# Optimization experiments

Hardware: AMD Instinct MI355X
Metric: run time of the kernel (lower is better)

## Reference

```python
import jax, jax.numpy as jnp
from jax import lax
import numpy as np

B, CIN, COUT, D, TDIM, E = 2, 16, 8, 96, 256, 8


def setup_inputs() -> dict:
    key = jax.random.key(0)
    ks = jax.random.split(key, 12)
    s = lambda fan: 1.0 / np.sqrt(fan)
    return {
        "x": jax.random.normal(ks[0], (B, CIN, D, D, D), jnp.float32),
        "text_features": jax.random.normal(ks[1], (B, TDIM), jnp.float32),
        # expert weight basis [E, Cout, Cin, 3, 3, 3] (kaiming-uniform-ish)
        "weight_basis": jax.random.uniform(ks[2], (E, COUT, CIN, 3, 3, 3), jnp.float32, -s(CIN * 27), s(CIN * 27)),
        "bias_basis": jnp.zeros((E, COUT), jnp.float32),
        # router MLP: text_dim -> 64 -> E
        "r_w1": jax.random.uniform(ks[3], (TDIM, 64), jnp.float32, -s(TDIM), s(TDIM)),
        "r_b1": jax.random.uniform(ks[4], (64,), jnp.float32, -s(TDIM), s(TDIM)),
        "r_w2": jax.random.uniform(ks[5], (64, E), jnp.float32, -s(64), s(64)),
        "r_b2": jax.random.uniform(ks[6], (E,), jnp.float32, -s(64), s(64)),
        # modulator MLP: text_dim -> 64 -> Cout
        "m_w1": jax.random.uniform(ks[7], (TDIM, 64), jnp.float32, -s(TDIM), s(TDIM)),
        "m_b1": jax.random.uniform(ks[8], (64,), jnp.float32, -s(TDIM), s(TDIM)),
        "m_w2": jax.random.uniform(ks[9], (64, COUT), jnp.float32, -s(64), s(64)),
        "m_b2": jax.random.uniform(ks[10], (COUT,), jnp.float32, -s(64), s(64)),
    }


def reference(x, text_features, weight_basis, bias_basis,
              r_w1, r_b1, r_w2, r_b2, m_w1, m_b1, m_w2, m_b2):
    b, cin = x.shape[0], x.shape[1]
    cout = weight_basis.shape[1]
    # router -> softmax routing weights over experts
    h = jax.nn.leaky_relu(text_features @ r_w1 + r_b1, 0.1)
    router_logits = h @ r_w2 + r_b2                      # [b, E]
    routing_weights = jax.nn.softmax(router_logits, -1)  # [b, E]
    # modulator -> per-sample channel gates
    g = jax.nn.leaky_relu(text_features @ m_w1 + m_b1, 0.1)
    gamma = jax.nn.sigmoid(g @ m_w2 + m_b2)              # [b, Cout]
    # per-sample dynamic conv weights via expert mixing
    cw = jnp.einsum('be,eoixyz->boixyz', routing_weights, weight_basis)  # [b,Cout,Cin,3,3,3]
    cb = routing_weights @ bias_basis                                    # [b, Cout]
    # grouped-conv trick: batch folded into channels, groups=b
    xr = x.reshape(1, b * cin, *x.shape[2:])
    wr = cw.reshape(b * cout, cin, 3, 3, 3)
    out = lax.conv_general_dilated(
        xr, wr, window_strides=(1, 1, 1), padding=[(1, 1)] * 3,
        dimension_numbers=('NCDHW', 'OIDHW', 'NCDHW'), feature_group_count=b)
    out = out.reshape(b, cout, *out.shape[2:]) + cb[:, :, None, None, None]
    out = out * (1.0 + gamma[:, :, None, None, None])
    return out, router_logits, routing_weights
```

## Files before the change

### kernel.cpp

```cpp
#include <hip/hip_runtime.h>
#include <math.h>

#define NB 2
#define CIN 16
#define COUT 8
#define DD 96
#define TDIM 256
#define NE 8
#define VOX (DD*DD*DD)
#define OUT_ELEMS (NB*COUT*VOX)

#define XT_BYTES ((size_t)NB * VOX * 32)
#define WS_A_F 7168
#define WS_D_F 7184

#define LX 18
#define PLANE (LX*LX)
#define NVX (PLANE*5)
#define HALFB (NVX*16)

#define NTB3 (VOX/512)

#define MWN (COUT*CIN*27)

typedef _Float16 f16x8 __attribute__((ext_vector_type(8)));
typedef _Float16 f16x4 __attribute__((ext_vector_type(4)));
typedef float f32x4 __attribute__((ext_vector_type(4)));

__global__ __launch_bounds__(256) void transpose_setup(
    const float* __restrict__ x, _Float16* __restrict__ xt,
    const float* __restrict__ text,
    const float* __restrict__ wb,
    const float* __restrict__ bb,
    const float* __restrict__ rw1, const float* __restrict__ rb1,
    const float* __restrict__ rw2, const float* __restrict__ rb2,
    const float* __restrict__ mw1, const float* __restrict__ mb1,
    const float* __restrict__ mw2, const float* __restrict__ mb2,
    float* __restrict__ dout_tail,
    char* __restrict__ tab)
{
    __shared__ struct {
        float mw[MWN];
        float part[256];
        float hg[2][64];
        float logits[NE];
        float rwv[NE];
    } s;
    const int t = threadIdx.x;
    const int b = blockIdx.y;

    if (blockIdx.x == NTB3) {
        {
            const int o = t & 127;
            const int which = o >> 6, j = o & 63;
            const int kh = t >> 7;
            const float* __restrict__ w1 = which ? mw1 : rw1;
            const float* __restrict__ tx = text + b*TDIM + kh*128;
            const float* __restrict__ wp = w1 + (size_t)(kh*128)*64 + j;
            float a0 = 0.f, a1 = 0.f, a2 = 0.f, a3 = 0.f;
            #pragma unroll 8
            for (int k = 0; k < 128; k += 4) {
                a0 = fmaf(tx[k+0], wp[(k+0)*64], a0);
                a1 = fmaf(tx[k+1], wp[(k+1)*64], a1);
                a2 = fmaf(tx[k+2], wp[(k+2)*64], a2);
                a3 = fmaf(tx[k+3], wp[(k+3)*64], a3);
            }
            s.part[t] = (a0 + a1) + (a2 + a3);
        }
        __syncthreads();
        if (t < 128) {
            const int which = t >> 6, j = t & 63;
            float acc = (which ? mb1 : rb1)[j] + s.part[t] + s.part[t + 128];
            s.hg[which][j] = (acc >= 0.f) ? acc : 0.1f * acc;
        }
        __syncthreads();
        if (t < NE) {
            float acc = rb2[t];
            #pragma unroll
            for (int k = 0; k < 64; ++k) acc = fmaf(s.hg[0][k], rw2[k*NE + t], acc);
            s.logits[t] = acc;
            dout_tail[b*NE + t] = acc;
        }
        __syncthreads();
        if (t < NE) {
            float mx = s.logits[0];
            for (int k = 1; k < NE; ++k) mx = fmaxf(mx, s.logits[k]);
            float ssum = 0.f;
            for (int k = 0; k < NE; ++k) ssum += expf(s.logits[k] - mx);
            const float w = expf(s.logits[t] - mx) / ssum;
            s.rwv[t] = w;
            dout_tail[NB*NE + b*NE + t] = w;
        }
        __syncthreads();
        float rv[NE];
        #pragma unroll
        for (int e = 0; e < NE; ++e) rv[e] = s.rwv[e];

        if (t < COUT) {
            float acc = mb2[t];
            #pragma unroll
            for (int k = 0; k < 64; ++k) acc = fmaf(s.hg[1][k], mw2[k*COUT + t], acc);
            const float gamma = 1.f / (1.f + expf(-acc));
            const float a = 1.f + gamma;
            float cb = 0.f;
            #pragma unroll
            for (int e = 0; e < NE; ++e) cb = fmaf(rv[e], bb[e*COUT + t], cb);
            ((float*)tab)[WS_A_F + b*COUT + t] = a;
            ((float*)tab)[WS_D_F + b*COUT + t] = cb * a;
        }

        #pragma unroll
        for (int i0 = 0; i0 < (MWN + 255)/256; ++i0) {
            const int i = i0*256 + t;
            if (i < MWN) {
                float v = 0.f;
                #pragma unroll
                for (int e = 0; e < NE; ++e) v = fmaf(rv[e], wb[e*MWN + i], v);
                s.mw[i] = v;
            }
        }
        __syncthreads();

        for (int r = t; r < 14*64*8; r += 256) {
            const int c  = r >> 9;
            const int l  = (r >> 3) & 63;
            const int j  = r & 7;
            const int q  = l >> 4;
            const int n  = l & 15;
            const int p  = q & 1;
            const int ci = (q >> 1)*8 + j;
            int tap;
            if (c < 9)        tap = (c/3)*9 + (c%3)*3 + p;
            else if (c < 12)  tap = (c-9)*9 + p*3 + 2;
            else if (c == 12) tap = p*9 + 8;
            else              tap = p ? -1 : 26;
            float v = 0.f;
            if (n < 8 && tap >= 0) v = s.mw[(n*CIN + ci)*27 + tap];
            ((_Float16*)tab)[b*7168 + r] = (_Float16)v;
        }
        return;
    }

    const int vh = blockIdx.x * 256 + t;
    const float* __restrict__ xb = x + (size_t)b * CIN * VOX;

    float2 f[CIN];
    #pragma unroll
    for (int ci = 0; ci < CIN; ++ci)
        f[ci] = ((const float2*)(xb + (size_t)ci * VOX))[vh];

    union { _Float16 h[16]; uint4 u[2]; } o0, o1;
    #pragma unroll
    for (int ci = 0; ci < CIN; ++ci) {
        o0.h[ci] = (_Float16)f[ci].x;
        o1.h[ci] = (_Float16)f[ci].y;
    }

    uint4* __restrict__ dst = (uint4*)(xt + (size_t)b * VOX * 16) + (size_t)vh * 4;
    dst[0] = o0.u[0];
    dst[1] = o0.u[1];
    dst[2] = o1.u[0];
    dst[3] = o1.u[1];
}

__global__ __launch_bounds__(256) void conv_mfma(
    const _Float16* __restrict__ xt,
    const char* __restrict__ tab,
    float* __restrict__ out)
{
    __shared__ char lds[2*HALFB];
    const int tid  = threadIdx.x;
    const int lane = tid & 63;
    const int wv   = tid >> 6;
    const int b    = blockIdx.z;
    const int z0   = blockIdx.y * 3;
    const int xti  = blockIdx.x % 6;
    const int yti  = blockIdx.x / 6;
    const int x0   = xti * 16, y0 = yti * 16;

    const f16x8* __restrict__ bfp = (const f16x8*)tab;
    f16x8 bfrag[14];
    #pragma unroll
    for (int c = 0; c < 14; ++c)
        bfrag[c] = bfp[(b*14 + c)*64 + lane];

    const _Float16* __restrict__ xtb = xt + (size_t)b * VOX * 16;
    for (int sv = tid; sv < NVX; sv += 256) {
        const int lz = sv / PLANE;
        const int r1 = sv - lz * PLANE;
        const int ly = r1 / LX;
        const int lx = r1 - ly * LX;
        const int zg = z0 - 1 + lz, yg = y0 - 1 + ly, xg = x0 - 1 + lx;
        const bool ok = ((unsigned)zg < 96u) & ((unsigned)yg < 96u) & ((unsigned)xg < 96u);
        const int zc = ok ? zg : 0, yc = ok ? yg : 0, xc = ok ? xg : 0;
        const uint4* __restrict__ p = (const uint4*)(xtb + (size_t)((zc*DD + yc)*DD + xc) * 16);
        uint4 lo = {0,0,0,0}, hi = {0,0,0,0};
        if (ok) { lo = p[0]; hi = p[1]; }
        *(uint4*)&lds[sv*16]         = lo;
        *(uint4*)&lds[HALFB + sv*16] = hi;
    }
    __syncthreads();

    const int q    = lane >> 4;
    const int m    = lane & 15;
    const int pbit = q & 1;
    const int hbit = q >> 1;

    const float* tabf = (const float*)tab;
    const float a_n = tabf[WS_A_F + b*8 + (m & 7)];
    const float d_n = tabf[WS_D_F + b*8 + (m & 7)];

    const int com = hbit*HALFB + m*16;
    const int dA = pbit*16;
    const int dB = pbit*288;
    const int dC = pbit*5184;

    #define LD_A(p_, dy_)  (*(const f16x8*)&lds[((p_)*PLANE + (yi+(dy_))*LX)*16 + com + dA])
    #define LD_G(p_)       (*(const f16x8*)&lds[((p_)*PLANE + yi*LX + 2)*16 + com + dB])
    #define LD_H12(zi_)    (*(const f16x8*)&lds[((zi_)*PLANE + (yi+2)*LX + 2)*16 + com + dC])
    #define LD_H13(zi_)    (*(const f16x8*)&lds[(((zi_)+2)*PLANE + (yi+2)*LX + 2)*16 + com])

    #pragma unroll
    for (int yi4 = 0; yi4 < 4; ++yi4) {
        const int yi = wv*4 + yi4;

        f16x8 A[3][3], G[3];
        #pragma unroll
        for (int dy = 0; dy < 3; ++dy) { A[0][dy] = LD_A(0, dy); A[1][dy] = LD_A(1, dy); }
        G[0] = LD_G(0); G[1] = LD_G(1);

        #pragma unroll
        for (int zi = 0; zi < 3; ++zi) {
            #pragma unroll
            for (int dy = 0; dy < 3; ++dy) A[2][dy] = LD_A(zi+2, dy);
            G[2] = LD_G(zi+2);
            const f16x8 H12v = LD_H12(zi);
            const f16x8 H13v = LD_H13(zi);

            f32x4 acc0 = {0.f,0.f,0.f,0.f}, acc1 = {0.f,0.f,0.f,0.f};
            acc0 = __builtin_amdgcn_mfma_f32_16x16x32_f16(A[0][0], bfrag[0],  acc0, 0,0,0);
            acc1 = __builtin_amdgcn_mfma_f32_16x16x32_f16(A[0][1], bfrag[1],  acc1, 0,0,0);
            acc0 = __builtin_amdgcn_mfma_f32_16x16x32_f16(A[0][2], bfrag[2],  acc0, 0,0,0);
            acc1 = __builtin_amdgcn_mfma_f32_16x16x32_f16(A[1][0], bfrag[3],  acc1, 0,0,0);
            acc0 = __builtin_amdgcn_mfma_f32_16x16x32_f16(A[1][1], bfrag[4],  acc0, 0,0,0);
            acc1 = __builtin_amdgcn_mfma_f32_16x16x32_f16(A[1][2], bfrag[5],  acc1, 0,0,0);
            acc0 = __builtin_amdgcn_mfma_f32_16x16x32_f16(A[2][0], bfrag[6],  acc0, 0,0,0);
            acc1 = __builtin_amdgcn_mfma_f32_16x16x32_f16(A[2][1], bfrag[7],  acc1, 0,0,0);
            acc0 = __builtin_amdgcn_mfma_f32_16x16x32_f16(A[2][2], bfrag[8],  acc0, 0,0,0);
            acc1 = __builtin_amdgcn_mfma_f32_16x16x32_f16(G[0],    bfrag[9],  acc1, 0,0,0);
            acc0 = __builtin_amdgcn_mfma_f32_16x16x32_f16(G[1],    bfrag[10], acc0, 0,0,0);
            acc1 = __builtin_amdgcn_mfma_f32_16x16x32_f16(G[2],    bfrag[11], acc1, 0,0,0);
            acc0 = __builtin_amdgcn_mfma_f32_16x16x32_f16(H12v,    bfrag[12], acc0, 0,0,0);
            acc1 = __builtin_amdgcn_mfma_f32_16x16x32_f16(H13v,    bfrag[13], acc1, 0,0,0);

            if (m < 8) {
                const int zz = z0 + zi, yy = y0 + yi;
                float* __restrict__ op = out + (size_t)(b*COUT + m)*VOX
                                            + (size_t)(zz*DD + yy)*DD + x0 + q*4;
                f32x4 res;
                #pragma unroll
                for (int r = 0; r < 4; ++r) res[r] = fmaf(acc0[r] + acc1[r], a_n, d_n);
                *reinterpret_cast<f32x4*>(op) = res;
            }

            #pragma unroll
            for (int dy = 0; dy < 3; ++dy) { A[0][dy] = A[1][dy]; A[1][dy] = A[2][dy]; }
            G[0] = G[1]; G[1] = G[2];
        }
    }
    #undef LD_A
    #undef LD_G
    #undef LD_H12
    #undef LD_H13
}

extern "C" void kernel_launch(void* const* d_in, const int* in_sizes, int n_in,
                              void* d_out, int out_size, void* d_ws, size_t ws_size,
                              hipStream_t stream) {
    const float* x    = (const float*)d_in[0];
    const float* text = (const float*)d_in[1];
    const float* wb   = (const float*)d_in[2];
    const float* bb   = (const float*)d_in[3];
    const float* rw1  = (const float*)d_in[4];
    const float* rb1  = (const float*)d_in[5];
    const float* rw2  = (const float*)d_in[6];
    const float* rb2  = (const float*)d_in[7];
    const float* mw1  = (const float*)d_in[8];
    const float* mb1  = (const float*)d_in[9];
    const float* mw2  = (const float*)d_in[10];
    const float* mb2  = (const float*)d_in[11];

    float* out = (float*)d_out;
    _Float16* xt = (_Float16*)d_ws;
    char* tab = (char*)d_ws + XT_BYTES;

    transpose_setup<<<dim3(NTB3 + 1, NB), 256, 0, stream>>>(
        x, xt, text, wb, bb, rw1, rb1, rw2, rb2, mw1, mb1, mw2, mb2,
        out + OUT_ELEMS, tab);

    conv_mfma<<<dim3(36, 32, NB), 256, 0, stream>>>(xt, tab, out);
}
```

Baseline: 249.7 us.

## Stream z-planes through an LDS ring buffer and fold the router into the conv kernel

The conv kernel now processes 12 output z-slices per block instead of 3. It keeps a 5-plane ring buffer in LDS, prefetching the next input plane into registers while computing the current one, which cuts halo reloads from 5 planes per 3 outputs to about 14 per 12. The router/modulator MLP and expert weight mixing move into every conv block, computed redundantly in LDS, so the separate setup block and the workspace table go away. The trade-off is a fixed per-block prologue (MLP plus mixing of about 27K weights), less parallelism from 4x fewer blocks, and a launch-bounds occupancy hint.

Result: no change. 252.2 us (+1.0%).

```diff
diff --git a/kernel.cpp b/kernel.cpp
--- a/kernel.cpp
+++ b/kernel.cpp
@@ -10,25 +10,48 @@
 #define VOX (DD*DD*DD)
 #define OUT_ELEMS (NB*COUT*VOX)
 
-#define XT_BYTES ((size_t)NB * VOX * 32)
-#define WS_A_F 7168
-#define WS_D_F 7184
-
 #define LX 18
 #define PLANE (LX*LX)
-#define NVX (PLANE*5)
+#define RING 5
+#define NVX (PLANE*RING)
 #define HALFB (NVX*16)
+#define ZCH 12
+#define NZB (DD/ZCH)
 
 #define NTB3 (VOX/512)
-
 #define MWN (COUT*CIN*27)
 
 typedef _Float16 f16x8 __attribute__((ext_vector_type(8)));
-typedef _Float16 f16x4 __attribute__((ext_vector_type(4)));
 typedef float f32x4 __attribute__((ext_vector_type(4)));
 
-__global__ __launch_bounds__(256) void transpose_setup(
-    const float* __restrict__ x, _Float16* __restrict__ xt,
+__global__ __launch_bounds__(256) void transpose_k(
+    const float* __restrict__ x, _Float16* __restrict__ xt)
+{
+    const int t = threadIdx.x;
+    const int b = blockIdx.y;
+    const int vh = blockIdx.x * 256 + t;
+    const float* __restrict__ xb = x + (size_t)b * CIN * VOX;
+
+    float2 f[CIN];
+    #pragma unroll
+    for (int ci = 0; ci < CIN; ++ci)
+        f[ci] = ((const float2*)(xb + (size_t)ci * VOX))[vh];
+
+    union { _Float16 h[16]; uint4 u[2]; } o0, o1;
+    #pragma unroll
+    for (int ci = 0; ci < CIN; ++ci) {
+        o0.h[ci] = (_Float16)f[ci].x;
+        o1.h[ci] = (_Float16)f[ci].y;
+    }
+    uint4* __restrict__ dst = (uint4*)(xt + (size_t)b * VOX * 16) + (size_t)vh * 4;
+    dst[0] = o0.u[0];
+    dst[1] = o0.u[1];
+    dst[2] = o1.u[0];
+    dst[3] = o1.u[1];
+}
+
+__global__ __launch_bounds__(256, 3) void conv_mfma(
+    const _Float16* __restrict__ xt,
     const float* __restrict__ text,
     const float* __restrict__ wb,
     const float* __restrict__ bb,
@@ -37,135 +60,6 @@
     const float* __restrict__ mw1, const float* __restrict__ mb1,
     const float* __restrict__ mw2, const float* __restrict__ mb2,
     float* __restrict__ dout_tail,
-    char* __restrict__ tab)
-{
-    __shared__ struct {
-        float mw[MWN];
-        float part[256];
-        float hg[2][64];
-        float logits[NE];
-        float rwv[NE];
-    } s;
-    const int t = threadIdx.x;
-    const int b = blockIdx.y;
-
-    if (blockIdx.x == NTB3) {
-        {
-            const int o = t & 127;
-            const int which = o >> 6, j = o & 63;
-            const int kh = t >> 7;
-            const float* __restrict__ w1 = which ? mw1 : rw1;
-            const float* __restrict__ tx = text + b*TDIM + kh*128;
-            const float* __restrict__ wp = w1 + (size_t)(kh*128)*64 + j;
-            float a0 = 0.f, a1 = 0.f, a2 = 0.f, a3 = 0.f;
-            #pragma unroll 8
-            for (int k = 0; k < 128; k += 4) {
-                a0 = fmaf(tx[k+0], wp[(k+0)*64], a0);
-                a1 = fmaf(tx[k+1], wp[(k+1)*64], a1);
-                a2 = fmaf(tx[k+2], wp[(k+2)*64], a2);
-                a3 = fmaf(tx[k+3], wp[(k+3)*64], a3);
-            }
-            s.part[t] = (a0 + a1) + (a2 + a3);
-        }
-        __syncthreads();
-        if (t < 128) {
-            const int which = t >> 6, j = t & 63;
-            float acc = (which ? mb1 : rb1)[j] + s.part[t] + s.part[t + 128];
-            s.hg[which][j] = (acc >= 0.f) ? acc : 0.1f * acc;
-        }
-        __syncthreads();
-        if (t < NE) {
-            float acc = rb2[t];
-            #pragma unroll
-            for (int k = 0; k < 64; ++k) acc = fmaf(s.hg[0][k], rw2[k*NE + t], acc);
-            s.logits[t] = acc;
-            dout_tail[b*NE + t] = acc;
-        }
-        __syncthreads();
-        if (t < NE) {
-            float mx = s.logits[0];
-            for (int k = 1; k < NE; ++k) mx = fmaxf(mx, s.logits[k]);
-            float ssum = 0.f;
-            for (int k = 0; k < NE; ++k) ssum += expf(s.logits[k] - mx);
-            const float w = expf(s.logits[t] - mx) / ssum;
-            s.rwv[t] = w;
-            dout_tail[NB*NE + b*NE + t] = w;
-        }
-        __syncthreads();
-        float rv[NE];
-        #pragma unroll
-        for (int e = 0; e < NE; ++e) rv[e] = s.rwv[e];
-
-        if (t < COUT) {
-            float acc = mb2[t];
-            #pragma unroll
-            for (int k = 0; k < 64; ++k) acc = fmaf(s.hg[1][k], mw2[k*COUT + t], acc);
-            const float gamma = 1.f / (1.f + expf(-acc));
-            const float a = 1.f + gamma;
-            float cb = 0.f;
-            #pragma unroll
-            for (int e = 0; e < NE; ++e) cb = fmaf(rv[e], bb[e*COUT + t], cb);
-            ((float*)tab)[WS_A_F + b*COUT + t] = a;
-            ((float*)tab)[WS_D_F + b*COUT + t] = cb * a;
-        }
-
-        #pragma unroll
-        for (int i0 = 0; i0 < (MWN + 255)/256; ++i0) {
-            const int i = i0*256 + t;
-            if (i < MWN) {
-                float v = 0.f;
-                #pragma unroll
-                for (int e = 0; e < NE; ++e) v = fmaf(rv[e], wb[e*MWN + i], v);
-                s.mw[i] = v;
-            }
-        }
-        __syncthreads();
-
-        for (int r = t; r < 14*64*8; r += 256) {
-            const int c  = r >> 9;
-            const int l  = (r >> 3) & 63;
-            const int j  = r & 7;
-            const int q  = l >> 4;
-            const int n  = l & 15;
-            const int p  = q & 1;
-            const int ci = (q >> 1)*8 + j;
-            int tap;
-            if (c < 9)        tap = (c/3)*9 + (c%3)*3 + p;
-            else if (c < 12)  tap = (c-9)*9 + p*3 + 2;
-            else if (c == 12) tap = p*9 + 8;
-            else              tap = p ? -1 : 26;
-            float v = 0.f;
-            if (n < 8 && tap >= 0) v = s.mw[(n*CIN + ci)*27 + tap];
-            ((_Float16*)tab)[b*7168 + r] = (_Float16)v;
-        }
-        return;
-    }
-
-    const int vh = blockIdx.x * 256 + t;
-    const float* __restrict__ xb = x + (size_t)b * CIN * VOX;
-
-    float2 f[CIN];
-    #pragma unroll
-    for (int ci = 0; ci < CIN; ++ci)
-        f[ci] = ((const float2*)(xb + (size_t)ci * VOX))[vh];
-
-    union { _Float16 h[16]; uint4 u[2]; } o0, o1;
-    #pragma unroll
-    for (int ci = 0; ci < CIN; ++ci) {
-        o0.h[ci] = (_Float16)f[ci].x;
-        o1.h[ci] = (_Float16)f[ci].y;
-    }
-
-    uint4* __restrict__ dst = (uint4*)(xt + (size_t)b * VOX * 16) + (size_t)vh * 4;
-    dst[0] = o0.u[0];
-    dst[1] = o0.u[1];
-    dst[2] = o1.u[0];
-    dst[3] = o1.u[1];
-}
-
-__global__ __launch_bounds__(256) void conv_mfma(
-    const _Float16* __restrict__ xt,
-    const char* __restrict__ tab,
     float* __restrict__ out)
 {
     __shared__ char lds[2*HALFB];
@@ -173,88 +67,189 @@
     const int lane = tid & 63;
     const int wv   = tid >> 6;
     const int b    = blockIdx.z;
-    const int z0   = blockIdx.y * 3;
+    const int zb   = blockIdx.y * ZCH;
     const int xti  = blockIdx.x % 6;
     const int yti  = blockIdx.x / 6;
     const int x0   = xti * 16, y0 = yti * 16;
-
-    const f16x8* __restrict__ bfp = (const f16x8*)tab;
+    const bool wr  = (blockIdx.x == 0) && (blockIdx.y == 0);
+
+    float* smw   = (float*)lds;
+    float* spart = (float*)(lds + 13824);
+    float* shg   = (float*)(lds + 14848);
+    float* slog  = (float*)(lds + 15360);
+    float* srwv  = (float*)(lds + 15392);
+    float* sa    = (float*)(lds + 15424);
+    float* sd    = (float*)(lds + 15456);
+
+    {
+        const int o = tid & 127, which = o >> 6, j = o & 63, kh = tid >> 7;
+        const float* __restrict__ w1 = which ? mw1 : rw1;
+        const float* __restrict__ tx = text + b*TDIM + kh*128;
+        const float* __restrict__ wp = w1 + (size_t)(kh*128)*64 + j;
+        float a0=0.f, a1=0.f, a2=0.f, a3=0.f;
+        #pragma unroll 8
+        for (int k = 0; k < 128; k += 4) {
+            a0 = fmaf(tx[k+0], wp[(k+0)*64], a0);
+            a1 = fmaf(tx[k+1], wp[(k+1)*64], a1);
+            a2 = fmaf(tx[k+2], wp[(k+2)*64], a2);
+            a3 = fmaf(tx[k+3], wp[(k+3)*64], a3);
+        }
+        spart[tid] = (a0 + a1) + (a2 + a3);
+    }
+    __syncthreads();
+    if (tid < 128) {
+        const int which = tid >> 6, j = tid & 63;
+        float acc = (which ? mb1 : rb1)[j] + spart[tid] + spart[tid + 128];
+        shg[which*64 + j] = (acc >= 0.f) ? acc : 0.1f * acc;
+    }
+    __syncthreads();
+    if (tid < NE) {
+        float acc = rb2[tid];
+        #pragma unroll
+        for (int k = 0; k < 64; ++k) acc = fmaf(shg[k], rw2[k*NE + tid], acc);
+        slog[tid] = acc;
+        if (wr) dout_tail[b*NE + tid] = acc;
+    }
+    __syncthreads();
+    if (tid < NE) {
+        float mx = slog[0];
+        for (int k = 1; k < NE; ++k) mx = fmaxf(mx, slog[k]);
+        float ssum = 0.f;
+        for (int k = 0; k < NE; ++k) ssum += expf(slog[k] - mx);
+        const float w = expf(slog[tid] - mx) / ssum;
+        srwv[tid] = w;
+        if (wr) dout_tail[NB*NE + b*NE + tid] = w;
+    }
+    __syncthreads();
+    float rv[NE];
+    #pragma unroll
+    for (int e = 0; e < NE; ++e) rv[e] = srwv[e];
+    if (tid < COUT) {
+        float acc = mb2[tid];
+        #pragma unroll
+        for (int k = 0; k < 64; ++k) acc = fmaf(shg[64 + k], mw2[k*COUT + tid], acc);
+        const float gamma = 1.f / (1.f + expf(-acc));
+        const float a = 1.f + gamma;
+        float cb = 0.f;
+        #pragma unroll
+        for (int e = 0; e < NE; ++e) cb = fmaf(rv[e], bb[e*COUT + tid], cb);
+        sa[tid] = a;
+        sd[tid] = cb * a;
+    }
+    #pragma unroll
+    for (int i0 = 0; i0 < (MWN + 255)/256; ++i0) {
+        const int i = i0*256 + tid;
+        if (i < MWN) {
+            float v = 0.f;
+            #pragma unroll
+            for (int e = 0; e < NE; ++e) v = fmaf(rv[e], wb[e*MWN + i], v);
+            smw[i] = v;
+        }
+    }
+    __syncthreads();
+
+    const int q = lane >> 4, m = lane & 15, pbit = q & 1, hbit = q >> 1;
     f16x8 bfrag[14];
-    #pragma unroll
-    for (int c = 0; c < 14; ++c)
-        bfrag[c] = bfp[(b*14 + c)*64 + lane];
+    {
+        const int cib = (q >> 1) * 8;
+        #pragma unroll
+        for (int c = 0; c < 14; ++c) {
+            int tap;
+            if (c < 9)        tap = (c/3)*9 + (c%3)*3 + pbit;
+            else if (c < 12)  tap = (c-9)*9 + pbit*3 + 2;
+            else if (c == 12) tap = pbit*9 + 8;
+            else              tap = pbit ? -1 : 26;
+            f16x8 v;
+            #pragma unroll
+            for (int j = 0; j < 8; ++j) v[j] = (_Float16)0.f;
+            if (m < 8 && tap >= 0) {
+                const float* mr = smw + (m*CIN + cib)*27 + tap;
+                #pragma unroll
+                for (int j = 0; j < 8; ++j) v[j] = (_Float16)mr[j*27];
+            }
+            bfrag[c] = v;
+        }
+    }
+    const float a_n = sa[m & 7];
+    const float d_n = sd[m & 7];
+    __syncthreads();
 
     const _Float16* __restrict__ xtb = xt + (size_t)b * VOX * 16;
-    for (int sv = tid; sv < NVX; sv += 256) {
-        const int lz = sv / PLANE;
-        const int r1 = sv - lz * PLANE;
-        const int ly = r1 / LX;
-        const int lx = r1 - ly * LX;
-        const int zg = z0 - 1 + lz, yg = y0 - 1 + ly, xg = x0 - 1 + lx;
-        const bool ok = ((unsigned)zg < 96u) & ((unsigned)yg < 96u) & ((unsigned)xg < 96u);
-        const int zc = ok ? zg : 0, yc = ok ? yg : 0, xc = ok ? xg : 0;
-        const uint4* __restrict__ p = (const uint4*)(xtb + (size_t)((zc*DD + yc)*DD + xc) * 16);
-        uint4 lo = {0,0,0,0}, hi = {0,0,0,0};
-        if (ok) { lo = p[0]; hi = p[1]; }
-        *(uint4*)&lds[sv*16]         = lo;
-        *(uint4*)&lds[HALFB + sv*16] = hi;
-    }
-    __syncthreads();
-
-    const int q    = lane >> 4;
-    const int m    = lane & 15;
-    const int pbit = q & 1;
-    const int hbit = q >> 1;
-
-    const float* tabf = (const float*)tab;
-    const float a_n = tabf[WS_A_F + b*8 + (m & 7)];
-    const float d_n = tabf[WS_D_F + b*8 + (m & 7)];
+    const int lyA = tid / LX, lxA = tid - lyA*LX;
+    const int ygA = y0 - 1 + lyA, xgA = x0 - 1 + lxA;
+    const bool okA = ((unsigned)ygA < 96u) & ((unsigned)xgA < 96u);
+    const int pvA = ygA*DD + xgA;
+    const int sB  = tid + 256;
+    const bool hasB = sB < PLANE;
+    const int lyB = sB / LX, lxB = sB - lyB*LX;
+    const int ygB = y0 - 1 + lyB, xgB = x0 - 1 + lxB;
+    const bool okB = hasB && (((unsigned)ygB < 96u) & ((unsigned)xgB < 96u));
+    const int pvB = ygB*DD + xgB;
+
+    #pragma unroll
+    for (int lp = 0; lp < 4; ++lp) {
+        const int zg = zb - 1 + lp;
+        const bool zok = (unsigned)zg < 96u;
+        uint4 l0 = make_uint4(0,0,0,0), h0 = l0, l1 = l0, h1 = l0;
+        if (okA && zok) { const uint4* p = (const uint4*)(xtb + ((size_t)zg*(DD*DD) + pvA)*16); l0 = p[0]; h0 = p[1]; }
+        if (okB && zok) { const uint4* p = (const uint4*)(xtb + ((size_t)zg*(DD*DD) + pvB)*16); l1 = p[0]; h1 = p[1]; }
+        *(uint4*)&lds[(lp*PLANE + tid)*16]          = l0;
+        *(uint4*)&lds[HALFB + (lp*PLANE + tid)*16]  = h0;
+        if (hasB) {
+            *(uint4*)&lds[(lp*PLANE + sB)*16]         = l1;
+            *(uint4*)&lds[HALFB + (lp*PLANE + sB)*16] = h1;
+        }
+    }
+    __syncthreads();
 
     const int com = hbit*HALFB + m*16;
     const int dA = pbit*16;
-    const int dB = pbit*288;
-    const int dC = pbit*5184;
-
-    #define LD_A(p_, dy_)  (*(const f16x8*)&lds[((p_)*PLANE + (yi+(dy_))*LX)*16 + com + dA])
-    #define LD_G(p_)       (*(const f16x8*)&lds[((p_)*PLANE + yi*LX + 2)*16 + com + dB])
-    #define LD_H12(zi_)    (*(const f16x8*)&lds[((zi_)*PLANE + (yi+2)*LX + 2)*16 + com + dC])
-    #define LD_H13(zi_)    (*(const f16x8*)&lds[(((zi_)+2)*PLANE + (yi+2)*LX + 2)*16 + com])
-
-    #pragma unroll
-    for (int yi4 = 0; yi4 < 4; ++yi4) {
-        const int yi = wv*4 + yi4;
-
-        f16x8 A[3][3], G[3];
-        #pragma unroll
-        for (int dy = 0; dy < 3; ++dy) { A[0][dy] = LD_A(0, dy); A[1][dy] = LD_A(1, dy); }
-        G[0] = LD_G(0); G[1] = LD_G(1);
-
-        #pragma unroll
-        for (int zi = 0; zi < 3; ++zi) {
-            #pragma unroll
-            for (int dy = 0; dy < 3; ++dy) A[2][dy] = LD_A(zi+2, dy);
-            G[2] = LD_G(zi+2);
-            const f16x8 H12v = LD_H12(zi);
-            const f16x8 H13v = LD_H13(zi);
+    const int dB = pbit*(LX*16);
+
+    #define LDV(sl_, vo_, dd_) (*(const f16x8*)&lds[((sl_)*PLANE + (vo_))*16 + com + (dd_)])
+
+    for (int zo = 0; zo < ZCH; ++zo) {
+        const bool st = (zo <= ZCH-3);
+        const int zgs = zb + zo + 3;
+        uint4 l0 = make_uint4(0,0,0,0), h0 = l0, l1 = l0, h1 = l0;
+        if (st) {
+            const bool zok = (unsigned)zgs < 96u;
+            if (okA && zok) { const uint4* p = (const uint4*)(xtb + ((size_t)zgs*(DD*DD) + pvA)*16); l0 = p[0]; h0 = p[1]; }
+            if (okB && zok) { const uint4* p = (const uint4*)(xtb + ((size_t)zgs*(DD*DD) + pvB)*16); l1 = p[0]; h1 = p[1]; }
+        }
+
+        const int s_0 = zo % RING, s_1 = (zo+1) % RING, s_2 = (zo+2) % RING;
+        const int sH12 = pbit ? s_1 : s_0;
+        const int sl0 = s_0, sl1 = s_1, sl2 = s_2;
+
+        #pragma unroll
+        for (int yi4 = 0; yi4 < 4; ++yi4) {
+            const int yi = wv*4 + yi4;
+            const f16x8 A00 = LDV(sl0, (yi+0)*LX, dA), A01 = LDV(sl0, (yi+1)*LX, dA), A02 = LDV(sl0, (yi+2)*LX, dA);
+            const f16x8 A10 = LDV(sl1, (yi+0)*LX, dA), A11 = LDV(sl1, (yi+1)*LX, dA), A12 = LDV(sl1, (yi+2)*LX, dA);
+            const f16x8 A20 = LDV(sl2, (yi+0)*LX, dA), A21 = LDV(sl2, (yi+1)*LX, dA), A22 = LDV(sl2, (yi+2)*LX, dA);
+            const f16x8 G0  = LDV(sl0, yi*LX + 2, dB), G1  = LDV(sl1, yi*LX + 2, dB), G2  = LDV(sl2, yi*LX + 2, dB);
+            const f16x8 H12v = LDV(sH12, (yi+2)*LX + 2, 0);
+            const f16x8 H13v = LDV(sl2,  (yi+2)*LX + 2, 0);
 
             f32x4 acc0 = {0.f,0.f,0.f,0.f}, acc1 = {0.f,0.f,0.f,0.f};
-            acc0 = __builtin_amdgcn_mfma_f32_16x16x32_f16(A[0][0], bfrag[0],  acc0, 0,0,0);
-            acc1 = __builtin_amdgcn_mfma_f32_16x16x32_f16(A[0][1], bfrag[1],  acc1, 0,0,0);
-            acc0 = __builtin_amdgcn_mfma_f32_16x16x32_f16(A[0][2], bfrag[2],  acc0, 0,0,0);
-            acc1 = __builtin_amdgcn_mfma_f32_16x16x32_f16(A[1][0], bfrag[3],  acc1, 0,0,0);
-            acc0 = __builtin_amdgcn_mfma_f32_16x16x32_f16(A[1][1], bfrag[4],  acc0, 0,0,0);
-            acc1 = __builtin_amdgcn_mfma_f32_16x16x32_f16(A[1][2], bfrag[5],  acc1, 0,0,0);
-            acc0 = __builtin_amdgcn_mfma_f32_16x16x32_f16(A[2][0], bfrag[6],  acc0, 0,0,0);
-            acc1 = __builtin_amdgcn_mfma_f32_16x16x32_f16(A[2][1], bfrag[7],  acc1, 0,0,0);
-            acc0 = __builtin_amdgcn_mfma_f32_16x16x32_f16(A[2][2], bfrag[8],  acc0, 0,0,0);
-            acc1 = __builtin_amdgcn_mfma_f32_16x16x32_f16(G[0],    bfrag[9],  acc1, 0,0,0);
-            acc0 = __builtin_amdgcn_mfma_f32_16x16x32_f16(G[1],    bfrag[10], acc0, 0,0,0);
-            acc1 = __builtin_amdgcn_mfma_f32_16x16x32_f16(G[2],    bfrag[11], acc1, 0,0,0);
-            acc0 = __builtin_amdgcn_mfma_f32_16x16x32_f16(H12v,    bfrag[12], acc0, 0,0,0);
-            acc1 = __builtin_amdgcn_mfma_f32_16x16x32_f16(H13v,    bfrag[13], acc1, 0,0,0);
+            acc0 = __builtin_amdgcn_mfma_f32_16x16x32_f16(A00,  bfrag[0],  acc0, 0,0,0);
+            acc1 = __builtin_amdgcn_mfma_f32_16x16x32_f16(A01,  bfrag[1],  acc1, 0,0,0);
+            acc0 = __builtin_amdgcn_mfma_f32_16x16x32_f16(A02,  bfrag[2],  acc0, 0,0,0);
+            acc1 = __builtin_amdgcn_mfma_f32_16x16x32_f16(A10,  bfrag[3],  acc1, 0,0,0);
+            acc0 = __builtin_amdgcn_mfma_f32_16x16x32_f16(A11,  bfrag[4],  acc0, 0,0,0);
+            acc1 = __builtin_amdgcn_mfma_f32_16x16x32_f16(A12,  bfrag[5],  acc1, 0,0,0);
+            acc0 = __builtin_amdgcn_mfma_f32_16x16x32_f16(A20,  bfrag[6],  acc0, 0,0,0);
+            acc1 = __builtin_amdgcn_mfma_f32_16x16x32_f16(A21,  bfrag[7],  acc1, 0,0,0);
+            acc0 = __builtin_amdgcn_mfma_f32_16x16x32_f16(A22,  bfrag[8],  acc0, 0,0,0);
+            acc1 = __builtin_amdgcn_mfma_f32_16x16x32_f16(G0,   bfrag[9],  acc1, 0,0,0);
+            acc0 = __builtin_amdgcn_mfma_f32_16x16x32_f16(G1,   bfrag[10], acc0, 0,0,0);
+            acc1 = __builtin_amdgcn_mfma_f32_16x16x32_f16(G2,   bfrag[11], acc1, 0,0,0);
+            acc0 = __builtin_amdgcn_mfma_f32_16x16x32_f16(H12v, bfrag[12], acc0, 0,0,0);
+            acc1 = __builtin_amdgcn_mfma_f32_16x16x32_f16(H13v, bfrag[13], acc1, 0,0,0);
 
             if (m < 8) {
-                const int zz = z0 + zi, yy = y0 + yi;
+                const int zz = zb + zo, yy = y0 + yi;
                 float* __restrict__ op = out + (size_t)(b*COUT + m)*VOX
                                             + (size_t)(zz*DD + yy)*DD + x0 + q*4;
                 f32x4 res;
@@ -262,16 +257,20 @@
                 for (int r = 0; r < 4; ++r) res[r] = fmaf(acc0[r] + acc1[r], a_n, d_n);
                 *reinterpret_cast<f32x4*>(op) = res;
             }
-
-            #pragma unroll
-            for (int dy = 0; dy < 3; ++dy) { A[0][dy] = A[1][dy]; A[1][dy] = A[2][dy]; }
-            G[0] = G[1]; G[1] = G[2];
-        }
-    }
-    #undef LD_A
-    #undef LD_G
-    #undef LD_H12
-    #undef LD_H13
+        }
+
+        if (st) {
+            const int sls = (zo+4) % RING;
+            *(uint4*)&lds[(sls*PLANE + tid)*16]          = l0;
+            *(uint4*)&lds[HALFB + (sls*PLANE + tid)*16]  = h0;
+            if (hasB) {
+                *(uint4*)&lds[(sls*PLANE + sB)*16]         = l1;
+                *(uint4*)&lds[HALFB + (sls*PLANE + sB)*16] = h1;
+            }
+        }
+        __syncthreads();
+    }
+    #undef LDV
 }
 
 extern "C" void kernel_launch(void* const* d_in, const int* in_sizes, int n_in,
@@ -292,11 +291,10 @@
 
     float* out = (float*)d_out;
     _Float16* xt = (_Float16*)d_ws;
-    char* tab = (char*)d_ws + XT_BYTES;
-
-    transpose_setup<<<dim3(NTB3 + 1, NB), 256, 0, stream>>>(
-        x, xt, text, wb, bb, rw1, rb1, rw2, rb2, mw1, mb1, mw2, mb2,
-        out + OUT_ELEMS, tab);
-
-    conv_mfma<<<dim3(36, 32, NB), 256, 0, stream>>>(xt, tab, out);
+
+    transpose_k<<<dim3(NTB3, NB), 256, 0, stream>>>(x, xt);
+
+    conv_mfma<<<dim3(36, NZB, NB), 256, 0, stream>>>(
+        xt, text, wb, bb, rw1, rb1, rw2, rb2, mw1, mb1, mw2, mb2,
+        out + OUT_ELEMS, out);
 }
```
